# Kernel optimization log

Measured on AMD Instinct MI355X. Metric: run time of the kernel, lower is better.

The kernel has to match this reference:

```python
import jax, jax.numpy as jnp
import numpy as np

BATCH, WIDTH, HEIGHT, DEPTH = 1024, 256, 256, 8


def setup_inputs() -> dict:
    key = jax.random.key(0)
    k_val, k_m1, k_b1, k_m2, k_b2 = jax.random.split(key, 5)
    return {
        "val": jax.random.normal(k_val, (BATCH, 1), dtype=jnp.float32),
        "M1": jax.random.normal(k_m1, (DEPTH, WIDTH, HEIGHT), dtype=jnp.float32),
        "B1": jax.random.normal(k_b1, (DEPTH, WIDTH, HEIGHT), dtype=jnp.float32),
        "M2": jax.random.normal(k_m2, (DEPTH, WIDTH, HEIGHT), dtype=jnp.float32),
        "B2": jax.random.normal(k_b2, (DEPTH, WIDTH, HEIGHT), dtype=jnp.float32),
    }


def _run_branch(q0, M, B):
    # q0: [B]; M, B: [depth, W, H]. Sequential recurrence over depth.
    def step(q, mb):
        m, b = mb  # [W, H]
        s = q[:, None, None] * m[None] + b[None]        # [B, W, H]
        q_new = jnp.min(jnp.max(s, axis=-1), axis=-1)    # max over H, then min over W -> [B]
        return q_new, None

    q_final, _ = jax.lax.scan(step, q0, (M, B))
    return q_final


def reference(val, M1, B1, M2, B2):
    q0 = val[:, 0]  # val: [B, 1] -> [B]
    q1 = _run_branch(q0, M1, B1)
    q2 = _run_branch(q0, M2, B2)
    return q1[:, None], q2[:, None]  # each [B, 1], matching torch squeeze(-1) of [B,1,1]
```

## Files before the change

kernel.cpp:

```cpp
#include <hip/hip_runtime.h>
#include <math.h>

#define WH     256
#define NDEPTH 8
#define NBATCH 1024
#define NB     8
#define PLANE  (WH * WH)

typedef _Float16 h2 __attribute__((ext_vector_type(2)));

#define HQBLK  (NDEPTH * 64 * WH)

__global__ __launch_bounds__(256) void transpose_half_k(const float* __restrict__ M1,
                                                        const float* __restrict__ B1,
                                                        const float* __restrict__ M2,
                                                        const float* __restrict__ B2,
                                                        _Float16* __restrict__ wsh) {
    __shared__ float tile[64][65];
    const int bid = blockIdx.x;
    const int arr = bid >> 7;
    const int d   = (bid >> 4) & 7;
    const int ht  = (bid >> 2) & 3;
    const int wt  = bid & 3;

    const float* src = (arr == 0) ? M1 : (arr == 1) ? B1 : (arr == 2) ? M2 : B2;
    const float* s = src + d * PLANE;
    _Float16* o = wsh + ((size_t)(arr * 4 + ht) * NDEPTH + d) * (64 * WH);

    const int t   = threadIdx.x;
    const int q16 = t >> 4;
    const int r16 = t & 15;

#pragma unroll
    for (int p = 0; p < 4; ++p) {
        const int wrow = q16 + p * 16;
        const float4 v = *(const float4*)(s + (wt * 64 + wrow) * WH + ht * 64 + r16 * 4);
        tile[wrow][r16 * 4 + 0] = v.x;
        tile[wrow][r16 * 4 + 1] = v.y;
        tile[wrow][r16 * 4 + 2] = v.z;
        tile[wrow][r16 * 4 + 3] = v.w;
    }
    __syncthreads();
#pragma unroll
    for (int p = 0; p < 4; ++p) {
        const int hrow = q16 + p * 16;
        const int wl   = r16 * 4;
        union { _Float16 f[4]; uint2 u; } pk;
        pk.f[0] = (_Float16)tile[wl + 0][hrow];
        pk.f[1] = (_Float16)tile[wl + 1][hrow];
        pk.f[2] = (_Float16)tile[wl + 2][hrow];
        pk.f[3] = (_Float16)tile[wl + 3][hrow];
        *(uint2*)(o + hrow * WH + wt * 64 + wl) = pk.u;
    }
}

__global__ __launch_bounds__(256) void prop_h_k(const _Float16* __restrict__ wsh,
                                                const float* __restrict__ val,
                                                float* __restrict__ out) {
    const int bid  = blockIdx.x;
    const int x    = bid & 7;
    const int br   = x >> 2;
    const int bg   = (bid >> 3) * 4 + (x & 3);
    const int t    = threadIdx.x;
    const int wave = t >> 6;
    const int lane = t & 63;

    const int arrM = br ? 2 : 0;
    const int arrB = br ? 3 : 1;
    const uint4* __restrict__ mp = (const uint4*)wsh + (size_t)(arrM * 4 + wave) * (HQBLK / 8) + lane;
    const uint4* __restrict__ bp = (const uint4*)wsh + (size_t)(arrB * 4 + wave) * (HQBLK / 8) + lane;

    h2 q2[NB];
#pragma unroll
    for (int nb = 0; nb < NB; ++nb) {
        const _Float16 qh = (_Float16)val[bg * NB + nb];
        q2[nb].x = qh; q2[nb].y = qh;
    }

    __shared__ h2 part[8][NB][128];
    __shared__ float qs[NB];

    union H8 { uint4 u; h2 h[4]; };

    uint4 bm[4][2], bb[4][2];
#pragma unroll
    for (int s = 0; s < 3; ++s) {
        bm[s][0] = mp[0]; bm[s][1] = mp[64];
        bb[s][0] = bp[0]; bb[s][1] = bp[64];
        mp += 128; bp += 128;
    }

    union { unsigned short us; _Float16 f; } ninf; ninf.us = 0xFC00;
    h2 NEGINF; NEGINF.x = ninf.f; NEGINF.y = ninf.f;

    for (int d = 0; d < NDEPTH; ++d) {
        h2 acc[NB][4];
#pragma unroll
        for (int nb = 0; nb < NB; ++nb)
#pragma unroll
            for (int k = 0; k < 4; ++k) acc[nb][k] = NEGINF;

#pragma unroll
        for (int c = 0; c < 16; ++c) {
            const int slot = c & 3;
            const int ps   = (c + 3) & 3;
            bm[ps][0] = mp[0]; bm[ps][1] = mp[64];
            bb[ps][0] = bp[0]; bb[ps][1] = bp[64];
            mp += 128; bp += 128;

            H8 m0, m1, b0, b1;
            m0.u = bm[slot][0]; m1.u = bm[slot][1];
            b0.u = bb[slot][0]; b1.u = bb[slot][1];
#pragma unroll
            for (int nb = 0; nb < NB; ++nb) {
                const h2 qq = q2[nb];
#pragma unroll
                for (int k = 0; k < 4; ++k) {
                    acc[nb][k] = __builtin_elementwise_max(
                        acc[nb][k], __builtin_elementwise_fma(qq, m0.h[k], b0.h[k]));
                    acc[nb][k] = __builtin_elementwise_max(
                        acc[nb][k], __builtin_elementwise_fma(qq, m1.h[k], b1.h[k]));
                }
            }
        }

        const int vw  = wave * 2 + (lane >> 5);
        const int j32 = lane & 31;
#pragma unroll
        for (int nb = 0; nb < NB; ++nb) {
            H8 st;
            st.h[0] = acc[nb][0]; st.h[1] = acc[nb][1];
            st.h[2] = acc[nb][2]; st.h[3] = acc[nb][3];
            *(uint4*)&part[vw][nb][j32 * 4] = st.u;
        }
        __syncthreads();

        {
            const int nb = t >> 5;
            const int j  = t & 31;
            H8 v; v.u = *(const uint4*)&part[0][nb][j * 4];
#pragma unroll
            for (int s2 = 1; s2 < 8; ++s2) {
                H8 w2; w2.u = *(const uint4*)&part[s2][nb][j * 4];
#pragma unroll
                for (int k = 0; k < 4; ++k)
                    v.h[k] = __builtin_elementwise_max(v.h[k], w2.h[k]);
            }
            h2 mn = __builtin_elementwise_min(
                        __builtin_elementwise_min(v.h[0], v.h[1]),
                        __builtin_elementwise_min(v.h[2], v.h[3]));
            float r = fminf((float)mn.x, (float)mn.y);
#pragma unroll
            for (int off = 16; off > 0; off >>= 1)
                r = fminf(r, __shfl_xor(r, off, 32));
            if (j == 0) qs[nb] = r;
        }
        __syncthreads();
#pragma unroll
        for (int nb = 0; nb < NB; ++nb) {
            const _Float16 qh = (_Float16)qs[nb];
            q2[nb].x = qh; q2[nb].y = qh;
        }
    }

    if (t < NB) out[br * NBATCH + bg * NB + t] = qs[t];
}

extern "C" void kernel_launch(void* const* d_in, const int* in_sizes, int n_in,
                              void* d_out, int out_size, void* d_ws, size_t ws_size,
                              hipStream_t stream) {
    const float* val = (const float*)d_in[0];
    const float* M1  = (const float*)d_in[1];
    const float* B1  = (const float*)d_in[2];
    const float* M2  = (const float*)d_in[3];
    const float* B2  = (const float*)d_in[4];
    float*    out = (float*)d_out;
    _Float16* wsh = (_Float16*)d_ws;

    transpose_half_k<<<dim3(512), dim3(256), 0, stream>>>(M1, B1, M2, B2, wsh);
    prop_h_k<<<dim3(256), dim3(256), 0, stream>>>(wsh, val, out);
}
```

Measured before the change: 112.4 us.

## Split H dimension across 8 waves per block with shuffle-based partial reduction

Re-lays the transposed half-precision weights into 32-row H slabs so each of 8 waves (512 threads) handles half the H range that a wave covered before. The per-wave loop shrinks from 16 to 8 chunks, and the two half-waves' partial maxima are merged with a cross-lane shuffle before writing shared memory. This doubles the waves per block to hide load latency and shorten the serial per-depth chain, at the cost of more registers per CU and larger block barriers.

Result: slower. 114.8 us (+2.2%).

```diff
diff --git a/kernel.cpp b/kernel.cpp
--- a/kernel.cpp
+++ b/kernel.cpp
@@ -9,7 +9,8 @@
 
 typedef _Float16 h2 __attribute__((ext_vector_type(2)));
 
-#define HQBLK  (NDEPTH * 64 * WH)
+#define SLAB   (32 * WH)
+#define HQ8BLK (NDEPTH * SLAB)
 
 __global__ __launch_bounds__(256) void transpose_half_k(const float* __restrict__ M1,
                                                         const float* __restrict__ B1,
@@ -25,7 +26,7 @@
 
     const float* src = (arr == 0) ? M1 : (arr == 1) ? B1 : (arr == 2) ? M2 : B2;
     const float* s = src + d * PLANE;
-    _Float16* o = wsh + ((size_t)(arr * 4 + ht) * NDEPTH + d) * (64 * WH);
+    _Float16* ob = wsh + (size_t)((arr * 8 + ht * 2) * NDEPTH + d) * SLAB;
 
     const int t   = threadIdx.x;
     const int q16 = t >> 4;
@@ -44,17 +45,19 @@
 #pragma unroll
     for (int p = 0; p < 4; ++p) {
         const int hrow = q16 + p * 16;
+        const int sub  = p >> 1;
+        const int hs   = q16 + (p & 1) * 16;
         const int wl   = r16 * 4;
         union { _Float16 f[4]; uint2 u; } pk;
         pk.f[0] = (_Float16)tile[wl + 0][hrow];
         pk.f[1] = (_Float16)tile[wl + 1][hrow];
         pk.f[2] = (_Float16)tile[wl + 2][hrow];
         pk.f[3] = (_Float16)tile[wl + 3][hrow];
-        *(uint2*)(o + hrow * WH + wt * 64 + wl) = pk.u;
+        *(uint2*)(ob + (size_t)sub * HQ8BLK + hs * WH + wt * 64 + wl) = pk.u;
     }
 }
 
-__global__ __launch_bounds__(256) void prop_h_k(const _Float16* __restrict__ wsh,
+__global__ __launch_bounds__(512) void prop_h_k(const _Float16* __restrict__ wsh,
                                                 const float* __restrict__ val,
                                                 float* __restrict__ out) {
     const int bid  = blockIdx.x;
@@ -67,8 +70,8 @@
 
     const int arrM = br ? 2 : 0;
     const int arrB = br ? 3 : 1;
-    const uint4* __restrict__ mp = (const uint4*)wsh + (size_t)(arrM * 4 + wave) * (HQBLK / 8) + lane;
-    const uint4* __restrict__ bp = (const uint4*)wsh + (size_t)(arrB * 4 + wave) * (HQBLK / 8) + lane;
+    const uint4* __restrict__ mp = (const uint4*)wsh + (size_t)(arrM * 8 + wave) * (HQ8BLK / 8) + lane;
+    const uint4* __restrict__ bp = (const uint4*)wsh + (size_t)(arrB * 8 + wave) * (HQ8BLK / 8) + lane;
 
     h2 q2[NB];
 #pragma unroll
@@ -101,7 +104,7 @@
             for (int k = 0; k < 4; ++k) acc[nb][k] = NEGINF;
 
 #pragma unroll
-        for (int c = 0; c < 16; ++c) {
+        for (int c = 0; c < 8; ++c) {
             const int slot = c & 3;
             const int ps   = (c + 3) & 3;
             bm[ps][0] = mp[0]; bm[ps][1] = mp[64];
@@ -124,18 +127,28 @@
             }
         }
 
-        const int vw  = wave * 2 + (lane >> 5);
-        const int j32 = lane & 31;
+        union IH { int i; h2 h; };
 #pragma unroll
-        for (int nb = 0; nb < NB; ++nb) {
-            H8 st;
-            st.h[0] = acc[nb][0]; st.h[1] = acc[nb][1];
-            st.h[2] = acc[nb][2]; st.h[3] = acc[nb][3];
-            *(uint4*)&part[vw][nb][j32 * 4] = st.u;
+        for (int nb = 0; nb < NB; ++nb)
+#pragma unroll
+            for (int k = 0; k < 4; ++k) {
+                IH a; a.h = acc[nb][k];
+                IH o2; o2.i = __shfl_xor(a.i, 32);
+                acc[nb][k] = __builtin_elementwise_max(acc[nb][k], o2.h);
+            }
+
+        if (lane < 32) {
+#pragma unroll
+            for (int nb = 0; nb < NB; ++nb) {
+                H8 st;
+                st.h[0] = acc[nb][0]; st.h[1] = acc[nb][1];
+                st.h[2] = acc[nb][2]; st.h[3] = acc[nb][3];
+                *(uint4*)&part[wave][nb][lane * 4] = st.u;
+            }
         }
         __syncthreads();
 
-        {
+        if (t < 256) {
             const int nb = t >> 5;
             const int j  = t & 31;
             H8 v; v.u = *(const uint4*)&part[0][nb][j * 4];
@@ -178,5 +191,5 @@
     _Float16* wsh = (_Float16*)d_ws;
 
     transpose_half_k<<<dim3(512), dim3(256), 0, stream>>>(M1, B1, M2, B2, wsh);
-    prop_h_k<<<dim3(256), dim3(256), 0, stream>>>(wsh, val, out);
+    prop_h_k<<<dim3(256), dim3(512), 0, stream>>>(wsh, val, out);
 }
```
